# Kernel optimization log

Measured on AMD Instinct MI355X. Metric: run time of the kernel, lower is better.

The kernel has to match this reference:

```python
import jax, jax.numpy as jnp
import numpy as np

B, L, H, E = 32, 128, 768, 64


def setup_inputs() -> dict:
    key = jax.random.key(0)
    ks = jax.random.split(key, 9)
    bert = jax.random.normal(ks[0], (B, L, H), jnp.float32)
    dep = jax.random.normal(ks[1], (B, L, L, E), jnp.float32)
    adj = jax.random.bernoulli(ks[2], 0.06, (B, L, L)).astype(jnp.int32)
    adj = adj.at[:, :, L - 1].set(0)  # avoid torch.roll wrap pairing edge case
    asp_start = jax.random.randint(ks[3], (B,), 1, L // 2)
    span = jax.random.randint(ks[4], (B,), 0, 4)
    asp_end = jnp.minimum(asp_start + span, L - 2)
    sc = 1.0 / np.sqrt(H).astype(np.float32)
    Wz = jax.random.normal(ks[5], (H, H), jnp.float32) * sc
    bz = jnp.zeros((H,), jnp.float32)
    wa = jax.random.normal(ks[6], (2 * H + E,), jnp.float32) * sc
    ba = jnp.zeros((), jnp.float32)
    Wf = jax.random.normal(ks[7], (H, H + E), jnp.float32) * sc
    Wh = jax.random.normal(ks[8], (H, 2 * H), jnp.float32) * sc
    return dict(bert_hidden_states=bert, dep_type_adj=dep, deprel_adj=adj,
                asp_start=asp_start, asp_end=asp_end,
                Wz=Wz, bz=bz, wa=wa, ba=ba, Wf=Wf, Wh=Wh)


def _forward(bert, dep, adj, asp_start, asp_end, Wz, bz, wa, ba, Wf, Wh):
    # z = z_linear(bert); zs[b, j] = z[b, j+1] (rolled-mask offset: adjacency idx j -> token j+1)
    z = bert @ Wz.T + bz
    zs = jnp.roll(z, -1, axis=1)                      # [B,L,H]
    wa_i, wa_j, wa_e = wa[:H], wa[H:2 * H], wa[2 * H:]
    s_i = zs @ wa_i                                    # [B,L] current-aspect term
    s_j = zs @ wa_j                                    # [B,L] neighbor term
    s_e = jnp.einsum('bije,e->bij', dep, wa_e)         # [B,L,L] dep-embed term
    score = jax.nn.leaky_relu(s_i[:, :, None] + s_j[:, None, :] + s_e + ba, 0.01)
    nb_mask = adj > 0                                  # [B,L,L]
    attn = jax.nn.softmax(jnp.where(nb_mask, score, -1e9), axis=-1)
    attn = jnp.where(nb_mask, attn, 0.0)
    # dep_type_fusion([neighbor, dep]) = zs @ Wf_z^T + dep @ Wf_e^T; weighted sum over j
    A = zs @ Wf[:, :H].T                               # [B,L,H]
    D = jnp.einsum('bij,bije->bie', attn, dep)         # [B,L,E]
    neighbor_repr = jnp.einsum('bij,bjh->bih', attn, A) + D @ Wf[:, H:].T  # [B,L,H]
    # w_h([neighbor_repr, current_asp_repr])
    temp = neighbor_repr @ Wh[:, :H].T + zs @ Wh[:, H:].T                   # [B,L,H]
    pos = jnp.arange(L)
    asp_valid = (pos[None, :] >= asp_start[:, None]) & (pos[None, :] <= asp_end[:, None])
    upd = asp_valid & nb_mask.any(-1)                  # update only aspects with >=1 neighbor
    # result for adjacency index i is written to token position i+1
    out = jnp.where(jnp.roll(upd, 1, axis=1)[:, :, None], jnp.roll(temp, 1, axis=1), bert)
    return out


def reference(bert_hidden_states, dep_type_adj, deprel_adj, asp_start, asp_end, Wz, bz, wa, ba, Wf, Wh):
    return _forward(bert_hidden_states, dep_type_adj, deprel_adj, asp_start, asp_end,
                    Wz, bz, wa, ba, Wf, Wh)
```

## Files before the change

kernel.cpp:

```cpp
#include <hip/hip_runtime.h>
#include <math.h>

#define NB 32
#define NL 128
#define NH 768
#define NE 64

#define OFF_ASLOT   32784
#define OFF_AIDX    49168
#define OFF_NASP    49680
#define OFF_AJCNT   49808
#define OFF_AJIDX   50320
#define OFF_RMAP    148624
#define OFF_BZD     155280
#define OFF_YB      155296
#define OFF_DG      548512
#define OFF_YP      581280
#define OFF_ZSAP    2154144
#define OFF_NBR     3727008
#define OFF_VIP     6872736
#define OFF_VJP     6897312

__global__ __launch_bounds__(256) void kA(
    const int* __restrict__ adj, const int* __restrict__ asp_s, const int* __restrict__ asp_e,
    const float* __restrict__ Wz, const float* __restrict__ wa, const float* __restrict__ bz,
    int* __restrict__ aspect_slot, int* __restrict__ aspect_idx, int* __restrict__ nasp,
    int* __restrict__ aj_cnt, int* __restrict__ aj_idx, int* __restrict__ row_map,
    float* __restrict__ viP, float* __restrict__ vjP, float* __restrict__ bzd,
    float* __restrict__ out) {
  int blk = blockIdx.x, tid = threadIdx.x;
  if (blk < 32) {
    int b = blk;
    __shared__ int asp_flag[128];
    __shared__ int s_aidx[4];
    __shared__ int s_nasp;
    if (tid < 128) {
      const int* arow = adj + ((size_t)(b * 128 + tid)) * 128;
      int any = 0;
      for (int j = 0; j < 128; j += 4) {
        int4 v = *(const int4*)(arow + j);
        any |= v.x | v.y | v.z | v.w;
      }
      int s0 = asp_s[b], e0 = asp_e[b];
      asp_flag[tid] = (tid >= s0 && tid <= e0 && any > 0) ? 1 : 0;
      aspect_slot[b * 128 + tid] = -1;
    }
    if (tid >= 128 && tid < 132) row_map[b * 4 + (tid - 128)] = b * 128;
    __syncthreads();
    if (tid == 0) {
      int n = 0;
      for (int i = 0; i < 128; ++i)
        if (asp_flag[i] && n < 4) s_aidx[n++] = i;
      s_nasp = n;
      nasp[b] = n;
    }
    __syncthreads();
    int w = tid >> 6, l = tid & 63;
    if (w < s_nasp) {
      int a = s_aidx[w];
      if (l == 0) {
        aspect_idx[b * 4 + w] = a;
        aspect_slot[b * 128 + a] = w;
        row_map[b * 4 + w] = b * 128 + a;
      }
      const int* ar = adj + ((size_t)(b * 128 + a)) * 128;
      int v0 = (ar[l] > 0) ? 1 : 0;
      int v1 = (ar[l + 64] > 0) ? 1 : 0;
      unsigned long long m0 = __ballot(v0);
      unsigned long long m1 = __ballot(v1);
      unsigned long long below = (1ull << l) - 1ull;
      int c0 = __popcll(m0 & below);
      int c1 = __popcll(m0) + __popcll(m1 & below);
      int* dst = aj_idx + (size_t)(b * 4 + w) * 128;
      if (v0) dst[c0] = l;
      if (v1) dst[c1] = l + 64;
      if (l == 0) aj_cnt[b * 4 + w] = __popcll(m0) + __popcll(m1);
    }
  } else if (blk < 56) {
    int idx = blk - 32;
    int kb = idx % 3, hb = idx / 3;
    int k = kb * 256 + tid;
    int h0 = hb * 96;
    float ai = 0.f, aj = 0.f;
#pragma unroll 8
    for (int h = h0; h < h0 + 96; ++h) {
      float w = Wz[(size_t)h * 768 + k];
      ai += w * wa[h];
      aj += w * wa[768 + h];
    }
    viP[hb * 768 + k] = ai;
    vjP[hb * 768 + k] = aj;
  } else if (blk == 56) {
    if (tid < 64) {
      float bi = 0.f, bj = 0.f;
#pragma unroll
      for (int q = 0; q < 12; ++q) {
        float bv = bz[q * 64 + tid];
        bi += bv * wa[q * 64 + tid];
        bj += bv * wa[768 + q * 64 + tid];
      }
#pragma unroll
      for (int d = 32; d; d >>= 1) { bi += __shfl_xor(bi, d, 64); bj += __shfl_xor(bj, d, 64); }
      if (tid == 0) { bzd[0] = bi; bzd[1] = bj; }
    }
  } else {
    int g = blk - 57;
    int b = g >> 2, s = g & 3;
    int s0 = asp_s[b], e0 = asp_e[b];
    __shared__ int flags[4];
    __shared__ int arow_sh;
    int w = tid >> 6, l = tid & 63;
    if (w < 4) {
      int row = s0 + w;
      int any = 0;
      if (row <= e0) {
        const int2* ar = (const int2*)(adj + ((size_t)(b * 128 + row)) * 128);
        int2 v = ar[l];
        unsigned long long m = __ballot((v.x | v.y) != 0);
        any = (m != 0ull) ? 1 : 0;
      }
      if (l == 0) flags[w] = any;
    }
    __syncthreads();
    if (tid == 0) {
      int n = 0, found = -1;
      for (int r = 0; r < 4 && s0 + r <= e0; ++r) {
        if (flags[r]) {
          if (n == s) { found = s0 + r; break; }
          ++n;
        }
      }
      arow_sh = found;
    }
    __syncthreads();
    int arow = arow_sh;
    if (arow >= 0 && tid < 192)
      ((float4*)out)[(size_t)(b * 128 + arow + 1) * 192 + tid] = make_float4(0.f, 0.f, 0.f, 0.f);
  }
}

__global__ __launch_bounds__(256) void kB(
    const float* __restrict__ dep, const float* __restrict__ bert,
    const float* __restrict__ wa, const float* __restrict__ ba,
    const float* __restrict__ viP, const float* __restrict__ vjP, const float* __restrict__ bzd,
    const float* __restrict__ Wz, const float* __restrict__ bz,
    const int* __restrict__ nasp, const int* __restrict__ aspect_idx,
    const int* __restrict__ aj_cnt, const int* __restrict__ aj_idx,
    const int* __restrict__ row_map,
    float* __restrict__ YB, float* __restrict__ DG, float* __restrict__ zsap) {
  int blk = blockIdx.x, tid = threadIdx.x;
  if (blk < 32) {
    int b = blk;
    int na = nasp[b];
    if (na == 0) return;
    __shared__ float vis[768];
    __shared__ float vjs[768];
    __shared__ float att[4][128];
    __shared__ float sjs[4][128];
    __shared__ float sis[4];
    __shared__ int jl[4][128];
    __shared__ int aidx[4];
    __shared__ int ajc[4];
    __shared__ float wae[64];
    if (tid < 4) { aidx[tid] = aspect_idx[b * 4 + tid]; ajc[tid] = aj_cnt[b * 4 + tid]; }
    if (tid < 64) wae[tid] = wa[1536 + tid];
    for (int q = tid; q < 512; q += 256) jl[q >> 7][q & 127] = aj_idx[b * 512 + q];
    for (int q = tid; q < 768; q += 256) {
      float a = 0.f, c = 0.f;
#pragma unroll
      for (int hb = 0; hb < 8; ++hb) { a += viP[hb * 768 + q]; c += vjP[hb * 768 + q]; }
      vis[q] = a;
      vjs[q] = c;
    }
    __syncthreads();
    int w = tid >> 6, l = tid & 63;
    float bzd0 = bzd[0], bzd1 = bzd[1];
    int offs[5];
    {
      int o = 0;
      for (int w2 = 0; w2 < 4; ++w2) { offs[w2] = o; if (w2 < na) o += 1 + ajc[w2]; }
      offs[4] = o;
    }
    for (int p = w; p < offs[4]; p += 4) {
      int w2 = 0;
      if (p >= offs[1]) w2 = 1;
      if (p >= offs[2]) w2 = 2;
      if (p >= offs[3]) w2 = 3;
      int idx = p - offs[w2];
      int row = (idx == 0) ? aidx[w2] : jl[w2][idx - 1];
      const float* br = bert + (size_t)(b * 128 + ((row + 1) & 127)) * 768;
      float acc = 0.f;
      if (idx == 0) {
#pragma unroll
        for (int q = 0; q < 12; ++q) acc += br[q * 64 + l] * vis[q * 64 + l];
      } else {
#pragma unroll
        for (int q = 0; q < 12; ++q) acc += br[q * 64 + l] * vjs[q * 64 + l];
      }
#pragma unroll
      for (int d = 32; d; d >>= 1) acc += __shfl_xor(acc, d, 64);
      if (l == 0) {
        if (idx == 0) sis[w2] = acc + bzd0;
        else sjs[w2][idx - 1] = acc + bzd1;
      }
    }
    __syncthreads();
    if (w >= na) return;
    int a = aidx[w], cj = ajc[w];
    float sib = sis[w] + ba[0];
    const float* depa = dep + ((size_t)(b * 128 + a)) * 128 * 64;
    float sc0 = -INFINITY, sc1 = -INFINITY;
    for (int t = l; t < cj; t += 64) {
      int j = jl[w][t];
      const float4* dp = (const float4*)(depa + (size_t)j * 64);
      float se = 0.f;
#pragma unroll
      for (int q = 0; q < 16; ++q) {
        float4 v = dp[q];
        se += v.x * wae[4 * q] + v.y * wae[4 * q + 1] + v.z * wae[4 * q + 2] + v.w * wae[4 * q + 3];
      }
      float sc = sib + sjs[w][t] + se;
      sc = (sc >= 0.f) ? sc : 0.01f * sc;
      if (t < 64) sc0 = sc; else sc1 = sc;
    }
    float mx = fmaxf(sc0, sc1);
#pragma unroll
    for (int d = 32; d; d >>= 1) mx = fmaxf(mx, __shfl_xor(mx, d, 64));
    float p0 = expf(sc0 - mx), p1 = expf(sc1 - mx);
    float sm = p0 + p1;
#pragma unroll
    for (int d = 32; d; d >>= 1) sm += __shfl_xor(sm, d, 64);
    float inv = 1.f / sm;
    if (l < cj) att[w][l] = p0 * inv;
    if (l + 64 < cj) att[w][l + 64] = p1 * inv;
    __syncthreads();
    float y[12];
#pragma unroll
    for (int q = 0; q < 12; ++q) y[q] = 0.f;
    float dacc = 0.f;
    int t = 0;
    for (; t + 4 <= cj; t += 4) {
      float a0 = att[w][t], a1 = att[w][t + 1], a2 = att[w][t + 2], a3 = att[w][t + 3];
      int j0 = jl[w][t], j1 = jl[w][t + 1], j2 = jl[w][t + 2], j3 = jl[w][t + 3];
      const float* br0 = bert + (size_t)(b * 128 + ((j0 + 1) & 127)) * 768;
      const float* br1 = bert + (size_t)(b * 128 + ((j1 + 1) & 127)) * 768;
      const float* br2 = bert + (size_t)(b * 128 + ((j2 + 1) & 127)) * 768;
      const float* br3 = bert + (size_t)(b * 128 + ((j3 + 1) & 127)) * 768;
      dacc += a0 * depa[(size_t)j0 * 64 + l] + a1 * depa[(size_t)j1 * 64 + l] +
              a2 * depa[(size_t)j2 * 64 + l] + a3 * depa[(size_t)j3 * 64 + l];
#pragma unroll
      for (int q = 0; q < 12; ++q)
        y[q] += a0 * br0[q * 64 + l] + a1 * br1[q * 64 + l] +
                a2 * br2[q * 64 + l] + a3 * br3[q * 64 + l];
    }
    for (; t < cj; ++t) {
      float at = att[w][t];
      int j = jl[w][t];
      const float* br = bert + (size_t)(b * 128 + ((j + 1) & 127)) * 768;
#pragma unroll
      for (int q = 0; q < 12; ++q) y[q] += at * br[q * 64 + l];
      dacc += at * depa[(size_t)j * 64 + l];
    }
    float* yr = YB + (size_t)(b * 4 + w) * 768;
#pragma unroll
    for (int q = 0; q < 12; ++q) yr[q * 64 + l] = y[q];
    DG[(b * 4 + w) * 64 + l] = dacc;
  } else {
    int idx = blk - 32;
    int kc = idx & 3, hc = (idx >> 2) % 3, bx = idx / 12;
    int s0 = bx * 4;
    __shared__ float Xs[4][192];
    if (tid < 192) {
      int r = tid / 48, c = tid - r * 48;
      int zrow = row_map[s0 + r];
      int bb = zrow >> 7, ii = zrow & 127;
      const float4* src = (const float4*)(bert + ((size_t)(bb * 128) + ((ii + 1) & 127)) * 768) + kc * 48;
      ((float4*)Xs[r])[c] = src[c];
    }
    __syncthreads();
    int h = hc * 256 + tid;
    const float4* wp = (const float4*)(Wz + (size_t)h * 768) + kc * 48;
    float accA[4] = {};
    float accB[4] = {};
#pragma unroll 6
    for (int k4 = 0; k4 < 24; ++k4) {
      float4 w0 = wp[k4];
      float4 w1 = wp[k4 + 24];
#pragma unroll
      for (int r = 0; r < 4; ++r) {
        float4 x0 = ((const float4*)Xs[r])[k4];
        float4 x1 = ((const float4*)Xs[r])[k4 + 24];
        accA[r] += x0.x * w0.x + x0.y * w0.y + x0.z * w0.z + x0.w * w0.w;
        accB[r] += x1.x * w1.x + x1.y * w1.y + x1.z * w1.z + x1.w * w1.w;
      }
    }
    float bzv = (kc == 0) ? bz[h] : 0.f;
#pragma unroll
    for (int r = 0; r < 4; ++r)
      zsap[((size_t)kc * 128 + s0 + r) * 768 + h] = accA[r] + accB[r] + bzv;
  }
}

__global__ __launch_bounds__(256) void kC(
    const float* __restrict__ YB, const float* __restrict__ DG, const float* __restrict__ zsap,
    const float* __restrict__ Wz, const float* __restrict__ bz,
    const float* __restrict__ Wf, const float* __restrict__ Wh,
    const int* __restrict__ row_map, const int* __restrict__ nasp,
    float* __restrict__ yp, float* __restrict__ NBR, float* __restrict__ out) {
  int blk = blockIdx.x, tid = threadIdx.x;
  __shared__ float Xs[4][192];
  if (blk < 384) {
    int kc = blk & 3, hc = (blk >> 2) % 3, bx = blk / 12;
    int s0 = bx * 4;
    if (tid < 192) {
      int r = tid / 48, c = tid - r * 48;
      const float4* src = (const float4*)(YB + (size_t)(s0 + r) * 768) + kc * 48;
      ((float4*)Xs[r])[c] = src[c];
    }
    __syncthreads();
    int h = hc * 256 + tid;
    const float4* wp = (const float4*)(Wz + (size_t)h * 768) + kc * 48;
    float accA[4] = {};
    float accB[4] = {};
#pragma unroll 6
    for (int k4 = 0; k4 < 24; ++k4) {
      float4 w0 = wp[k4];
      float4 w1 = wp[k4 + 24];
#pragma unroll
      for (int r = 0; r < 4; ++r) {
        float4 x0 = ((const float4*)Xs[r])[k4];
        float4 x1 = ((const float4*)Xs[r])[k4 + 24];
        accA[r] += x0.x * w0.x + x0.y * w0.y + x0.z * w0.z + x0.w * w0.w;
        accB[r] += x1.x * w1.x + x1.y * w1.y + x1.z * w1.z + x1.w * w1.w;
      }
    }
    float bzv = (kc == 0) ? bz[h] : 0.f;
#pragma unroll
    for (int r = 0; r < 4; ++r)
      yp[((size_t)kc * 128 + s0 + r) * 768 + h] = accA[r] + accB[r] + bzv;
  } else if (blk < 768) {
    int idx = blk - 384;
    int kc2 = idx & 3, nc = (idx >> 2) % 3, g = idx / 12;
    if (tid < 192) {
      int r = tid / 48, c = tid - r * 48;
      int row = g * 4 + r;
      int Q = kc2 * 48 + c;
      float4 p0 = *((const float4*)(zsap + (size_t)row * 768) + Q);
      float4 p1 = *((const float4*)(zsap + ((size_t)128 + row) * 768) + Q);
      float4 p2 = *((const float4*)(zsap + ((size_t)256 + row) * 768) + Q);
      float4 p3 = *((const float4*)(zsap + ((size_t)384 + row) * 768) + Q);
      ((float4*)Xs[r])[c] = make_float4(p0.x + p1.x + p2.x + p3.x, p0.y + p1.y + p2.y + p3.y,
                                        p0.z + p1.z + p2.z + p3.z, p0.w + p1.w + p2.w + p3.w);
    }
    __syncthreads();
    int h = nc * 256 + tid;
    float acc[4] = {};
    const float4* wp = (const float4*)(Wh + (size_t)h * 1536 + 768 + kc2 * 192);
#pragma unroll 4
    for (int k4 = 0; k4 < 48; ++k4) {
      float4 wv = wp[k4];
#pragma unroll
      for (int r = 0; r < 4; ++r) {
        float4 xv = ((const float4*)Xs[r])[k4];
        acc[r] += xv.x * wv.x + xv.y * wv.y + xv.z * wv.z + xv.w * wv.w;
      }
    }
#pragma unroll
    for (int r = 0; r < 4; ++r) {
      int row = g * 4 + r;
      int b = row >> 2, s = row & 3;
      if (s < nasp[b]) {
        int orow = row_map[row] + 1;
        atomicAdd(&out[(size_t)orow * 768 + h], acc[r]);
      }
    }
  } else {
    int idx = blk - 768;
    int nc = idx % 3, g = idx / 3;
    if (tid < 64) {
      int r = tid / 16, c = tid - r * 16;
      ((float4*)Xs[r])[c] = *((const float4*)(DG + (size_t)(g * 4 + r) * 64) + c);
    }
    __syncthreads();
    int h = nc * 256 + tid;
    float acc[4] = {};
    const float4* wp = (const float4*)(Wf + (size_t)h * 832 + 768);
#pragma unroll
    for (int k4 = 0; k4 < 16; ++k4) {
      float4 wv = wp[k4];
#pragma unroll
      for (int r = 0; r < 4; ++r) {
        float4 xv = ((const float4*)Xs[r])[k4];
        acc[r] += xv.x * wv.x + xv.y * wv.y + xv.z * wv.z + xv.w * wv.w;
      }
    }
#pragma unroll
    for (int r = 0; r < 4; ++r)
      NBR[(size_t)(g * 4 + r) * 768 + h] = acc[r];
  }
}

__global__ __launch_bounds__(256) void kD(
    const float* __restrict__ yp, const float* __restrict__ Wf,
    float* __restrict__ NBR) {
  int blk = blockIdx.x, tid = threadIdx.x;
  int kc = blk & 3, nc = (blk >> 2) % 3, g = blk / 12;
  __shared__ float Xs[4][192];
  if (tid < 192) {
    int r = tid / 48, c = tid - r * 48;
    int row = g * 4 + r;
    int Q = kc * 48 + c;
    float4 p0 = *((const float4*)(yp + (size_t)row * 768) + Q);
    float4 p1 = *((const float4*)(yp + ((size_t)128 + row) * 768) + Q);
    float4 p2 = *((const float4*)(yp + ((size_t)256 + row) * 768) + Q);
    float4 p3 = *((const float4*)(yp + ((size_t)384 + row) * 768) + Q);
    ((float4*)Xs[r])[c] = make_float4(p0.x + p1.x + p2.x + p3.x, p0.y + p1.y + p2.y + p3.y,
                                      p0.z + p1.z + p2.z + p3.z, p0.w + p1.w + p2.w + p3.w);
  }
  __syncthreads();
  int h = nc * 256 + tid;
  float acc[4] = {};
  const float4* wp = (const float4*)(Wf + (size_t)h * 832 + kc * 192);
#pragma unroll 4
  for (int k4 = 0; k4 < 48; ++k4) {
    float4 wv = wp[k4];
#pragma unroll
    for (int r = 0; r < 4; ++r) {
      float4 xv = ((const float4*)Xs[r])[k4];
      acc[r] += xv.x * wv.x + xv.y * wv.y + xv.z * wv.z + xv.w * wv.w;
    }
  }
#pragma unroll
  for (int r = 0; r < 4; ++r)
    atomicAdd(&NBR[(size_t)(g * 4 + r) * 768 + h], acc[r]);
}

__global__ __launch_bounds__(256) void kE(
    const float* __restrict__ NBR, const float* __restrict__ Wh,
    const int* __restrict__ row_map, const int* __restrict__ nasp,
    const int* __restrict__ adj, const int* __restrict__ asp_s, const int* __restrict__ asp_e,
    const float* __restrict__ bert,
    float* __restrict__ out) {
  int blk = blockIdx.x, tid = threadIdx.x;
  if (blk < 384) {
    int kc = blk & 3, nc = (blk >> 2) % 3, g = blk / 12;
    __shared__ float Xs[4][192];
    if (tid < 192) {
      int r = tid / 48, c = tid - r * 48;
      ((float4*)Xs[r])[c] = *((const float4*)(NBR + (size_t)(g * 4 + r) * 768 + kc * 192) + c);
    }
    __syncthreads();
    int h = nc * 256 + tid;
    float acc[4] = {};
    const float4* wp = (const float4*)(Wh + (size_t)h * 1536 + kc * 192);
#pragma unroll 4
    for (int k4 = 0; k4 < 48; ++k4) {
      float4 wv = wp[k4];
#pragma unroll
      for (int r = 0; r < 4; ++r) {
        float4 xv = ((const float4*)Xs[r])[k4];
        acc[r] += xv.x * wv.x + xv.y * wv.y + xv.z * wv.z + xv.w * wv.w;
      }
    }
#pragma unroll
    for (int r = 0; r < 4; ++r) {
      int row = g * 4 + r;
      int b = row >> 2, s = row & 3;
      if (s < nasp[b]) {
        int orow = row_map[row] + 1;
        atomicAdd(&out[(size_t)orow * 768 + h], acc[r]);
      }
    }
  } else {
    int row = blk - 384;
    int b = row >> 7, i = row & 127;
    __shared__ int s_upd;
    if (tid == 0) s_upd = 0;
    __syncthreads();
    if (i > 0) {
      int ip = i - 1;
      int s0 = asp_s[b], e0 = asp_e[b];
      if (ip >= s0 && ip <= e0 && tid < 64) {
        const int2* ar = (const int2*)(adj + ((size_t)(b * 128 + ip)) * 128);
        int2 v = ar[tid];
        unsigned long long m = __ballot((v.x | v.y) != 0);
        if (tid == 0 && m != 0ull) s_upd = 1;
      }
    }
    __syncthreads();
    if (!s_upd && tid < 192)
      ((float4*)out)[(size_t)row * 192 + tid] = ((const float4*)bert)[(size_t)row * 192 + tid];
  }
}

extern "C" void kernel_launch(void* const* d_in, const int* in_sizes, int n_in,
                              void* d_out, int out_size, void* d_ws, size_t ws_size,
                              hipStream_t stream) {
  const float* bert = (const float*)d_in[0];
  const float* dep  = (const float*)d_in[1];
  const int*   adj  = (const int*)d_in[2];
  const int*   asps = (const int*)d_in[3];
  const int*   aspe = (const int*)d_in[4];
  const float* Wz   = (const float*)d_in[5];
  const float* bz   = (const float*)d_in[6];
  const float* wa   = (const float*)d_in[7];
  const float* ba   = (const float*)d_in[8];
  const float* Wf   = (const float*)d_in[9];
  const float* Wh   = (const float*)d_in[10];
  float* out = (float*)d_out;
  char* ws = (char*)d_ws;

  int*   aspect_slot = (int*)(ws + OFF_ASLOT);
  int*   aspect_idx  = (int*)(ws + OFF_AIDX);
  int*   nasp        = (int*)(ws + OFF_NASP);
  int*   aj_cnt      = (int*)(ws + OFF_AJCNT);
  int*   aj_idx      = (int*)(ws + OFF_AJIDX);
  int*   row_map     = (int*)(ws + OFF_RMAP);
  float* bzd         = (float*)(ws + OFF_BZD);
  float* YB          = (float*)(ws + OFF_YB);
  float* DG          = (float*)(ws + OFF_DG);
  float* yp          = (float*)(ws + OFF_YP);
  float* zsap        = (float*)(ws + OFF_ZSAP);
  float* NBR         = (float*)(ws + OFF_NBR);
  float* viP         = (float*)(ws + OFF_VIP);
  float* vjP         = (float*)(ws + OFF_VJP);

  kA<<<185, 256, 0, stream>>>(adj, asps, aspe, Wz, wa, bz,
                              aspect_slot, aspect_idx, nasp, aj_cnt, aj_idx, row_map,
                              viP, vjP, bzd, out);
  kB<<<416, 256, 0, stream>>>(dep, bert, wa, ba, viP, vjP, bzd, Wz, bz,
                              nasp, aspect_idx, aj_cnt, aj_idx, row_map,
                              YB, DG, zsap);
  kC<<<864, 256, 0, stream>>>(YB, DG, zsap, Wz, bz, Wf, Wh, row_map, nasp, yp, NBR, out);
  kD<<<384, 256, 0, stream>>>(yp, Wf, NBR);
  kE<<<4480, 256, 0, stream>>>(NBR, Wh, row_map, nasp, adj, asps, aspe, bert, out);
}
```

Baseline: 87.07 us.

## Fuse setup kernel into attention kernel and recompute projections per block

The separate preprocessing kernel is removed and its work moves into the attention kernel. Each per-batch block now builds its own aspect and neighbor lists, the folded Wz·wa vectors and the bias dot products in shared memory, so the global round-trips and one launch go away. The z-projection blocks rebuild the aspect row map locally instead of reading it from the workspace. In exchange, every per-batch block reads all of Wz serially to form vi/vj, which was previously split across 24 blocks. That adds a long per-block critical path. The barrier between the attention-weight write and its read inside a wave is also dropped.

Measured after the change: 155.5 us. 1.79x slower.

```diff
diff --git a/kernel.cpp b/kernel.cpp
--- a/kernel.cpp
+++ b/kernel.cpp
@@ -6,34 +6,38 @@
 #define NH 768
 #define NE 64
 
-#define OFF_ASLOT   32784
-#define OFF_AIDX    49168
 #define OFF_NASP    49680
-#define OFF_AJCNT   49808
-#define OFF_AJIDX   50320
 #define OFF_RMAP    148624
-#define OFF_BZD     155280
 #define OFF_YB      155296
 #define OFF_DG      548512
 #define OFF_YP      581280
 #define OFF_ZSAP    2154144
 #define OFF_NBR     3727008
-#define OFF_VIP     6872736
-#define OFF_VJP     6897312
-
-__global__ __launch_bounds__(256) void kA(
+
+__global__ __launch_bounds__(256) void kB(
     const int* __restrict__ adj, const int* __restrict__ asp_s, const int* __restrict__ asp_e,
-    const float* __restrict__ Wz, const float* __restrict__ wa, const float* __restrict__ bz,
-    int* __restrict__ aspect_slot, int* __restrict__ aspect_idx, int* __restrict__ nasp,
-    int* __restrict__ aj_cnt, int* __restrict__ aj_idx, int* __restrict__ row_map,
-    float* __restrict__ viP, float* __restrict__ vjP, float* __restrict__ bzd,
+    const float* __restrict__ dep, const float* __restrict__ bert,
+    const float* __restrict__ wa, const float* __restrict__ ba,
+    const float* __restrict__ Wz, const float* __restrict__ bz,
+    int* __restrict__ nasp, int* __restrict__ row_map,
+    float* __restrict__ YB, float* __restrict__ DG, float* __restrict__ zsap,
     float* __restrict__ out) {
   int blk = blockIdx.x, tid = threadIdx.x;
   if (blk < 32) {
     int b = blk;
+    __shared__ float vis[768];
+    __shared__ float vjs[768];
+    __shared__ float att[4][128];
+    __shared__ float sjs[4][128];
+    __shared__ float sis[4];
+    __shared__ int jl[4][128];
+    __shared__ int aidx[4];
+    __shared__ int ajc[4];
+    __shared__ float wae[64];
     __shared__ int asp_flag[128];
     __shared__ int s_aidx[4];
     __shared__ int s_nasp;
+    __shared__ float bzd_sh[2];
     if (tid < 128) {
       const int* arow = adj + ((size_t)(b * 128 + tid)) * 128;
       int any = 0;
@@ -43,9 +47,8 @@
       }
       int s0 = asp_s[b], e0 = asp_e[b];
       asp_flag[tid] = (tid >= s0 && tid <= e0 && any > 0) ? 1 : 0;
-      aspect_slot[b * 128 + tid] = -1;
-    }
-    if (tid >= 128 && tid < 132) row_map[b * 4 + (tid - 128)] = b * 128;
+    }
+    if (tid >= 128 && tid < 192) wae[tid - 128] = wa[1536 + (tid - 128)];
     __syncthreads();
     if (tid == 0) {
       int n = 0;
@@ -54,15 +57,16 @@
       s_nasp = n;
       nasp[b] = n;
     }
-    __syncthreads();
+    if (tid == 1) {
+      row_map[b * 4 + 0] = b * 128; row_map[b * 4 + 1] = b * 128;
+      row_map[b * 4 + 2] = b * 128; row_map[b * 4 + 3] = b * 128;
+    }
+    __syncthreads();
+    int na = s_nasp;
     int w = tid >> 6, l = tid & 63;
-    if (w < s_nasp) {
+    if (w < na) {
       int a = s_aidx[w];
-      if (l == 0) {
-        aspect_idx[b * 4 + w] = a;
-        aspect_slot[b * 128 + a] = w;
-        row_map[b * 4 + w] = b * 128 + a;
-      }
+      if (l == 0) { aidx[w] = a; row_map[b * 4 + w] = b * 128 + a; }
       const int* ar = adj + ((size_t)(b * 128 + a)) * 128;
       int v0 = (ar[l] > 0) ? 1 : 0;
       int v1 = (ar[l + 64] > 0) ? 1 : 0;
@@ -71,26 +75,25 @@
       unsigned long long below = (1ull << l) - 1ull;
       int c0 = __popcll(m0 & below);
       int c1 = __popcll(m0) + __popcll(m1 & below);
-      int* dst = aj_idx + (size_t)(b * 4 + w) * 128;
-      if (v0) dst[c0] = l;
-      if (v1) dst[c1] = l + 64;
-      if (l == 0) aj_cnt[b * 4 + w] = __popcll(m0) + __popcll(m1);
-    }
-  } else if (blk < 56) {
-    int idx = blk - 32;
-    int kb = idx % 3, hb = idx / 3;
-    int k = kb * 256 + tid;
-    int h0 = hb * 96;
-    float ai = 0.f, aj = 0.f;
-#pragma unroll 8
-    for (int h = h0; h < h0 + 96; ++h) {
-      float w = Wz[(size_t)h * 768 + k];
-      ai += w * wa[h];
-      aj += w * wa[768 + h];
-    }
-    viP[hb * 768 + k] = ai;
-    vjP[hb * 768 + k] = aj;
-  } else if (blk == 56) {
+      if (v0) jl[w][c0] = l;
+      if (v1) jl[w][c1] = l + 64;
+      if (l == 0) ajc[w] = __popcll(m0) + __popcll(m1);
+    }
+    if (w == 3 || (na == 0 && w == 0)) {
+    }
+    {
+      float ai0 = 0.f, ai1 = 0.f, ai2 = 0.f, aj0 = 0.f, aj1 = 0.f, aj2 = 0.f;
+#pragma unroll 4
+      for (int h = 0; h < 768; ++h) {
+        float whi = wa[h], whj = wa[768 + h];
+        const float* wr = Wz + (size_t)h * 768;
+        float w0 = wr[tid], w1 = wr[tid + 256], w2 = wr[tid + 512];
+        ai0 += w0 * whi; ai1 += w1 * whi; ai2 += w2 * whi;
+        aj0 += w0 * whj; aj1 += w1 * whj; aj2 += w2 * whj;
+      }
+      vis[tid] = ai0; vis[tid + 256] = ai1; vis[tid + 512] = ai2;
+      vjs[tid] = aj0; vjs[tid + 256] = aj1; vjs[tid + 512] = aj2;
+    }
     if (tid < 64) {
       float bi = 0.f, bj = 0.f;
 #pragma unroll
@@ -101,10 +104,158 @@
       }
 #pragma unroll
       for (int d = 32; d; d >>= 1) { bi += __shfl_xor(bi, d, 64); bj += __shfl_xor(bj, d, 64); }
-      if (tid == 0) { bzd[0] = bi; bzd[1] = bj; }
-    }
+      if (tid == 0) { bzd_sh[0] = bi; bzd_sh[1] = bj; }
+    }
+    __syncthreads();
+    if (na == 0) return;
+    float bzd0 = bzd_sh[0], bzd1 = bzd_sh[1];
+    int offs[5];
+    {
+      int o = 0;
+      for (int w2 = 0; w2 < 4; ++w2) { offs[w2] = o; if (w2 < na) o += 1 + ajc[w2]; }
+      offs[4] = o;
+    }
+    for (int p = w; p < offs[4]; p += 4) {
+      int w2 = 0;
+      if (p >= offs[1]) w2 = 1;
+      if (p >= offs[2]) w2 = 2;
+      if (p >= offs[3]) w2 = 3;
+      int idx = p - offs[w2];
+      int row = (idx == 0) ? aidx[w2] : jl[w2][idx - 1];
+      const float* br = bert + (size_t)(b * 128 + ((row + 1) & 127)) * 768;
+      float acc = 0.f;
+      if (idx == 0) {
+#pragma unroll
+        for (int q = 0; q < 12; ++q) acc += br[q * 64 + l] * vis[q * 64 + l];
+      } else {
+#pragma unroll
+        for (int q = 0; q < 12; ++q) acc += br[q * 64 + l] * vjs[q * 64 + l];
+      }
+#pragma unroll
+      for (int d = 32; d; d >>= 1) acc += __shfl_xor(acc, d, 64);
+      if (l == 0) {
+        if (idx == 0) sis[w2] = acc + bzd0;
+        else sjs[w2][idx - 1] = acc + bzd1;
+      }
+    }
+    __syncthreads();
+    if (w >= na) return;
+    int a = aidx[w], cj = ajc[w];
+    float sib = sis[w] + ba[0];
+    const float* depa = dep + ((size_t)(b * 128 + a)) * 128 * 64;
+    float sc0 = -INFINITY, sc1 = -INFINITY;
+    for (int t = l; t < cj; t += 64) {
+      int j = jl[w][t];
+      const float4* dp = (const float4*)(depa + (size_t)j * 64);
+      float se = 0.f;
+#pragma unroll
+      for (int q = 0; q < 16; ++q) {
+        float4 v = dp[q];
+        se += v.x * wae[4 * q] + v.y * wae[4 * q + 1] + v.z * wae[4 * q + 2] + v.w * wae[4 * q + 3];
+      }
+      float sc = sib + sjs[w][t] + se;
+      sc = (sc >= 0.f) ? sc : 0.01f * sc;
+      if (t < 64) sc0 = sc; else sc1 = sc;
+    }
+    float mx = fmaxf(sc0, sc1);
+#pragma unroll
+    for (int d = 32; d; d >>= 1) mx = fmaxf(mx, __shfl_xor(mx, d, 64));
+    float p0 = expf(sc0 - mx), p1 = expf(sc1 - mx);
+    float sm = p0 + p1;
+#pragma unroll
+    for (int d = 32; d; d >>= 1) sm += __shfl_xor(sm, d, 64);
+    float inv = 1.f / sm;
+    if (l < cj) att[w][l] = p0 * inv;
+    if (l + 64 < cj) att[w][l + 64] = p1 * inv;
+    float y[12];
+#pragma unroll
+    for (int q = 0; q < 12; ++q) y[q] = 0.f;
+    float dacc = 0.f;
+    int t = 0;
+    for (; t + 4 <= cj; t += 4) {
+      float a0 = att[w][t], a1 = att[w][t + 1], a2 = att[w][t + 2], a3 = att[w][t + 3];
+      int j0 = jl[w][t], j1 = jl[w][t + 1], j2 = jl[w][t + 2], j3 = jl[w][t + 3];
+      const float* br0 = bert + (size_t)(b * 128 + ((j0 + 1) & 127)) * 768;
+      const float* br1 = bert + (size_t)(b * 128 + ((j1 + 1) & 127)) * 768;
+      const float* br2 = bert + (size_t)(b * 128 + ((j2 + 1) & 127)) * 768;
+      const float* br3 = bert + (size_t)(b * 128 + ((j3 + 1) & 127)) * 768;
+      dacc += a0 * depa[(size_t)j0 * 64 + l] + a1 * depa[(size_t)j1 * 64 + l] +
+              a2 * depa[(size_t)j2 * 64 + l] + a3 * depa[(size_t)j3 * 64 + l];
+#pragma unroll
+      for (int q = 0; q < 12; ++q)
+        y[q] += a0 * br0[q * 64 + l] + a1 * br1[q * 64 + l] +
+                a2 * br2[q * 64 + l] + a3 * br3[q * 64 + l];
+    }
+    for (; t < cj; ++t) {
+      float at = att[w][t];
+      int j = jl[w][t];
+      const float* br = bert + (size_t)(b * 128 + ((j + 1) & 127)) * 768;
+#pragma unroll
+      for (int q = 0; q < 12; ++q) y[q] += at * br[q * 64 + l];
+      dacc += at * depa[(size_t)j * 64 + l];
+    }
+    float* yr = YB + (size_t)(b * 4 + w) * 768;
+#pragma unroll
+    for (int q = 0; q < 12; ++q) yr[q * 64 + l] = y[q];
+    DG[(b * 4 + w) * 64 + l] = dacc;
+  } else if (blk < 416) {
+    int idx = blk - 32;
+    int kc = idx & 3, hc = (idx >> 2) % 3, bx = idx / 12;
+    int b = bx;
+    __shared__ int rmap_loc[4];
+    __shared__ int flags[4];
+    __shared__ float Xs[4][192];
+    int s0a = asp_s[b], e0a = asp_e[b];
+    int w = tid >> 6, l = tid & 63;
+    if (w < 4) {
+      int row = s0a + w;
+      int any = 0;
+      if (row <= e0a) {
+        const int2* ar = (const int2*)(adj + ((size_t)(b * 128 + row)) * 128);
+        int2 v = ar[l];
+        unsigned long long m = __ballot((v.x | v.y) != 0);
+        any = (m != 0ull) ? 1 : 0;
+      }
+      if (l == 0) flags[w] = any;
+    }
+    __syncthreads();
+    if (tid == 0) {
+      rmap_loc[0] = rmap_loc[1] = rmap_loc[2] = rmap_loc[3] = b * 128;
+      int n = 0;
+      for (int r = 0; r < 4 && s0a + r <= e0a; ++r)
+        if (flags[r] && n < 4) rmap_loc[n++] = b * 128 + (s0a + r);
+    }
+    __syncthreads();
+    if (tid < 192) {
+      int r = tid / 48, c = tid - r * 48;
+      int zrow = rmap_loc[r];
+      int bb = zrow >> 7, ii = zrow & 127;
+      const float4* src = (const float4*)(bert + ((size_t)(bb * 128) + ((ii + 1) & 127)) * 768) + kc * 48;
+      ((float4*)Xs[r])[c] = src[c];
+    }
+    __syncthreads();
+    int h = hc * 256 + tid;
+    const float4* wp = (const float4*)(Wz + (size_t)h * 768) + kc * 48;
+    float accA[4] = {};
+    float accB[4] = {};
+#pragma unroll 6
+    for (int k4 = 0; k4 < 24; ++k4) {
+      float4 w0 = wp[k4];
+      float4 w1 = wp[k4 + 24];
+#pragma unroll
+      for (int r = 0; r < 4; ++r) {
+        float4 x0 = ((const float4*)Xs[r])[k4];
+        float4 x1 = ((const float4*)Xs[r])[k4 + 24];
+        accA[r] += x0.x * w0.x + x0.y * w0.y + x0.z * w0.z + x0.w * w0.w;
+        accB[r] += x1.x * w1.x + x1.y * w1.y + x1.z * w1.z + x1.w * w1.w;
+      }
+    }
+    float bzv = (kc == 0) ? bz[h] : 0.f;
+#pragma unroll
+    for (int r = 0; r < 4; ++r)
+      zsap[((size_t)kc * 128 + (bx * 4) + r) * 768 + h] = accA[r] + accB[r] + bzv;
   } else {
-    int g = blk - 57;
+    int g = blk - 416;
     int b = g >> 2, s = g & 3;
     int s0 = asp_s[b], e0 = asp_e[b];
     __shared__ int flags[4];
@@ -136,168 +287,6 @@
     int arow = arow_sh;
     if (arow >= 0 && tid < 192)
       ((float4*)out)[(size_t)(b * 128 + arow + 1) * 192 + tid] = make_float4(0.f, 0.f, 0.f, 0.f);
-  }
-}
-
-__global__ __launch_bounds__(256) void kB(
-    const float* __restrict__ dep, const float* __restrict__ bert,
-    const float* __restrict__ wa, const float* __restrict__ ba,
-    const float* __restrict__ viP, const float* __restrict__ vjP, const float* __restrict__ bzd,
-    const float* __restrict__ Wz, const float* __restrict__ bz,
-    const int* __restrict__ nasp, const int* __restrict__ aspect_idx,
-    const int* __restrict__ aj_cnt, const int* __restrict__ aj_idx,
-    const int* __restrict__ row_map,
-    float* __restrict__ YB, float* __restrict__ DG, float* __restrict__ zsap) {
-  int blk = blockIdx.x, tid = threadIdx.x;
-  if (blk < 32) {
-    int b = blk;
-    int na = nasp[b];
-    if (na == 0) return;
-    __shared__ float vis[768];
-    __shared__ float vjs[768];
-    __shared__ float att[4][128];
-    __shared__ float sjs[4][128];
-    __shared__ float sis[4];
-    __shared__ int jl[4][128];
-    __shared__ int aidx[4];
-    __shared__ int ajc[4];
-    __shared__ float wae[64];
-    if (tid < 4) { aidx[tid] = aspect_idx[b * 4 + tid]; ajc[tid] = aj_cnt[b * 4 + tid]; }
-    if (tid < 64) wae[tid] = wa[1536 + tid];
-    for (int q = tid; q < 512; q += 256) jl[q >> 7][q & 127] = aj_idx[b * 512 + q];
-    for (int q = tid; q < 768; q += 256) {
-      float a = 0.f, c = 0.f;
-#pragma unroll
-      for (int hb = 0; hb < 8; ++hb) { a += viP[hb * 768 + q]; c += vjP[hb * 768 + q]; }
-      vis[q] = a;
-      vjs[q] = c;
-    }
-    __syncthreads();
-    int w = tid >> 6, l = tid & 63;
-    float bzd0 = bzd[0], bzd1 = bzd[1];
-    int offs[5];
-    {
-      int o = 0;
-      for (int w2 = 0; w2 < 4; ++w2) { offs[w2] = o; if (w2 < na) o += 1 + ajc[w2]; }
-      offs[4] = o;
-    }
-    for (int p = w; p < offs[4]; p += 4) {
-      int w2 = 0;
-      if (p >= offs[1]) w2 = 1;
-      if (p >= offs[2]) w2 = 2;
-      if (p >= offs[3]) w2 = 3;
-      int idx = p - offs[w2];
-      int row = (idx == 0) ? aidx[w2] : jl[w2][idx - 1];
-      const float* br = bert + (size_t)(b * 128 + ((row + 1) & 127)) * 768;
-      float acc = 0.f;
-      if (idx == 0) {
-#pragma unroll
-        for (int q = 0; q < 12; ++q) acc += br[q * 64 + l] * vis[q * 64 + l];
-      } else {
-#pragma unroll
-        for (int q = 0; q < 12; ++q) acc += br[q * 64 + l] * vjs[q * 64 + l];
-      }
-#pragma unroll
-      for (int d = 32; d; d >>= 1) acc += __shfl_xor(acc, d, 64);
-      if (l == 0) {
-        if (idx == 0) sis[w2] = acc + bzd0;
-        else sjs[w2][idx - 1] = acc + bzd1;
-      }
-    }
-    __syncthreads();
-    if (w >= na) return;
-    int a = aidx[w], cj = ajc[w];
-    float sib = sis[w] + ba[0];
-    const float* depa = dep + ((size_t)(b * 128 + a)) * 128 * 64;
-    float sc0 = -INFINITY, sc1 = -INFINITY;
-    for (int t = l; t < cj; t += 64) {
-      int j = jl[w][t];
-      const float4* dp = (const float4*)(depa + (size_t)j * 64);
-      float se = 0.f;
-#pragma unroll
-      for (int q = 0; q < 16; ++q) {
-        float4 v = dp[q];
-        se += v.x * wae[4 * q] + v.y * wae[4 * q + 1] + v.z * wae[4 * q + 2] + v.w * wae[4 * q + 3];
-      }
-      float sc = sib + sjs[w][t] + se;
-      sc = (sc >= 0.f) ? sc : 0.01f * sc;
-      if (t < 64) sc0 = sc; else sc1 = sc;
-    }
-    float mx = fmaxf(sc0, sc1);
-#pragma unroll
-    for (int d = 32; d; d >>= 1) mx = fmaxf(mx, __shfl_xor(mx, d, 64));
-    float p0 = expf(sc0 - mx), p1 = expf(sc1 - mx);
-    float sm = p0 + p1;
-#pragma unroll
-    for (int d = 32; d; d >>= 1) sm += __shfl_xor(sm, d, 64);
-    float inv = 1.f / sm;
-    if (l < cj) att[w][l] = p0 * inv;
-    if (l + 64 < cj) att[w][l + 64] = p1 * inv;
-    __syncthreads();
-    float y[12];
-#pragma unroll
-    for (int q = 0; q < 12; ++q) y[q] = 0.f;
-    float dacc = 0.f;
-    int t = 0;
-    for (; t + 4 <= cj; t += 4) {
-      float a0 = att[w][t], a1 = att[w][t + 1], a2 = att[w][t + 2], a3 = att[w][t + 3];
-      int j0 = jl[w][t], j1 = jl[w][t + 1], j2 = jl[w][t + 2], j3 = jl[w][t + 3];
-      const float* br0 = bert + (size_t)(b * 128 + ((j0 + 1) & 127)) * 768;
-      const float* br1 = bert + (size_t)(b * 128 + ((j1 + 1) & 127)) * 768;
-      const float* br2 = bert + (size_t)(b * 128 + ((j2 + 1) & 127)) * 768;
-      const float* br3 = bert + (size_t)(b * 128 + ((j3 + 1) & 127)) * 768;
-      dacc += a0 * depa[(size_t)j0 * 64 + l] + a1 * depa[(size_t)j1 * 64 + l] +
-              a2 * depa[(size_t)j2 * 64 + l] + a3 * depa[(size_t)j3 * 64 + l];
-#pragma unroll
-      for (int q = 0; q < 12; ++q)
-        y[q] += a0 * br0[q * 64 + l] + a1 * br1[q * 64 + l] +
-                a2 * br2[q * 64 + l] + a3 * br3[q * 64 + l];
-    }
-    for (; t < cj; ++t) {
-      float at = att[w][t];
-      int j = jl[w][t];
-      const float* br = bert + (size_t)(b * 128 + ((j + 1) & 127)) * 768;
-#pragma unroll
-      for (int q = 0; q < 12; ++q) y[q] += at * br[q * 64 + l];
-      dacc += at * depa[(size_t)j * 64 + l];
-    }
-    float* yr = YB + (size_t)(b * 4 + w) * 768;
-#pragma unroll
-    for (int q = 0; q < 12; ++q) yr[q * 64 + l] = y[q];
-    DG[(b * 4 + w) * 64 + l] = dacc;
-  } else {
-    int idx = blk - 32;
-    int kc = idx & 3, hc = (idx >> 2) % 3, bx = idx / 12;
-    int s0 = bx * 4;
-    __shared__ float Xs[4][192];
-    if (tid < 192) {
-      int r = tid / 48, c = tid - r * 48;
-      int zrow = row_map[s0 + r];
-      int bb = zrow >> 7, ii = zrow & 127;
-      const float4* src = (const float4*)(bert + ((size_t)(bb * 128) + ((ii + 1) & 127)) * 768) + kc * 48;
-      ((float4*)Xs[r])[c] = src[c];
-    }
-    __syncthreads();
-    int h = hc * 256 + tid;
-    const float4* wp = (const float4*)(Wz + (size_t)h * 768) + kc * 48;
-    float accA[4] = {};
-    float accB[4] = {};
-#pragma unroll 6
-    for (int k4 = 0; k4 < 24; ++k4) {
-      float4 w0 = wp[k4];
-      float4 w1 = wp[k4 + 24];
-#pragma unroll
-      for (int r = 0; r < 4; ++r) {
-        float4 x0 = ((const float4*)Xs[r])[k4];
-        float4 x1 = ((const float4*)Xs[r])[k4 + 24];
-        accA[r] += x0.x * w0.x + x0.y * w0.y + x0.z * w0.z + x0.w * w0.w;
-        accB[r] += x1.x * w1.x + x1.y * w1.y + x1.z * w1.z + x1.w * w1.w;
-      }
-    }
-    float bzv = (kc == 0) ? bz[h] : 0.f;
-#pragma unroll
-    for (int r = 0; r < 4; ++r)
-      zsap[((size_t)kc * 128 + s0 + r) * 768 + h] = accA[r] + accB[r] + bzv;
   }
 }
 
@@ -510,27 +499,16 @@
   float* out = (float*)d_out;
   char* ws = (char*)d_ws;
 
-  int*   aspect_slot = (int*)(ws + OFF_ASLOT);
-  int*   aspect_idx  = (int*)(ws + OFF_AIDX);
-  int*   nasp        = (int*)(ws + OFF_NASP);
-  int*   aj_cnt      = (int*)(ws + OFF_AJCNT);
-  int*   aj_idx      = (int*)(ws + OFF_AJIDX);
-  int*   row_map     = (int*)(ws + OFF_RMAP);
-  float* bzd         = (float*)(ws + OFF_BZD);
-  float* YB          = (float*)(ws + OFF_YB);
-  float* DG          = (float*)(ws + OFF_DG);
-  float* yp          = (float*)(ws + OFF_YP);
-  float* zsap        = (float*)(ws + OFF_ZSAP);
-  float* NBR         = (float*)(ws + OFF_NBR);
-  float* viP         = (float*)(ws + OFF_VIP);
-  float* vjP         = (float*)(ws + OFF_VJP);
-
-  kA<<<185, 256, 0, stream>>>(adj, asps, aspe, Wz, wa, bz,
-                              aspect_slot, aspect_idx, nasp, aj_cnt, aj_idx, row_map,
-                              viP, vjP, bzd, out);
-  kB<<<416, 256, 0, stream>>>(dep, bert, wa, ba, viP, vjP, bzd, Wz, bz,
-                              nasp, aspect_idx, aj_cnt, aj_idx, row_map,
-                              YB, DG, zsap);
+  int*   nasp     = (int*)(ws + OFF_NASP);
+  int*   row_map  = (int*)(ws + OFF_RMAP);
+  float* YB       = (float*)(ws + OFF_YB);
+  float* DG       = (float*)(ws + OFF_DG);
+  float* yp       = (float*)(ws + OFF_YP);
+  float* zsap     = (float*)(ws + OFF_ZSAP);
+  float* NBR      = (float*)(ws + OFF_NBR);
+
+  kB<<<544, 256, 0, stream>>>(adj, asps, aspe, dep, bert, wa, ba, Wz, bz,
+                              nasp, row_map, YB, DG, zsap, out);
   kC<<<864, 256, 0, stream>>>(YB, DG, zsap, Wz, bz, Wf, Wh, row_map, nasp, yp, NBR, out);
   kD<<<384, 256, 0, stream>>>(yp, Wf, NBR);
   kE<<<4480, 256, 0, stream>>>(NBR, Wh, row_map, nasp, adj, asps, aspe, bert, out);
```
